# Performance work log

Measured on AMD Instinct MI355X. Metric: run time of the kernel, lower is better.

## Reference

```python
import jax, jax.numpy as jnp
import numpy as np

N = 100000
E = 3200000
IN_C, HID, OUT_C = 256, 32, 16


def gcn_conv(x, W, b, src, dst, n):
    """PyG GCNConv: h = D^{-1/2}(A+I)D^{-1/2} (x W) + b, self-loops already in src/dst."""
    h = x @ W  # [N, out]
    deg = jax.ops.segment_sum(jnp.ones_like(dst, dtype=h.dtype), dst, num_segments=n)
    dinv = jax.lax.rsqrt(deg)  # deg >= 1 because of self-loops
    norm = dinv[src] * dinv[dst]  # [E_all]
    msg = h[src] * norm[:, None]  # gather + normalize
    return jax.ops.segment_sum(msg, dst, num_segments=n) + b


def setup_inputs() -> dict:
    key = jax.random.key(0)
    k1, k2, k3, k4 = jax.random.split(key, 4)
    x = jax.random.normal(k1, (N, IN_C), dtype=jnp.float32)
    edge_index = jax.random.randint(k2, (2, E), 0, N, dtype=jnp.int64)
    # Glorot-ish init for weights, zero bias (as in PyG defaults)
    W1 = jax.random.normal(k3, (IN_C, HID), dtype=jnp.float32) / np.sqrt(IN_C)
    b1 = jnp.zeros((HID,), dtype=jnp.float32)
    W2 = jax.random.normal(k4, (HID, OUT_C), dtype=jnp.float32) / np.sqrt(HID)
    b2 = jnp.zeros((OUT_C,), dtype=jnp.float32)
    return {"x": x, "edge_index": edge_index, "W1": W1, "b1": b1, "W2": W2, "b2": b2}


def reference(x, edge_index, W1, b1, W2, b2):
    n = x.shape[0]
    loops = jnp.arange(n, dtype=edge_index.dtype)
    src = jnp.concatenate([edge_index[0], loops])  # add self-loops
    dst = jnp.concatenate([edge_index[1], loops])
    h = jax.nn.relu(gcn_conv(x, W1, b1, src, dst, n))
    return gcn_conv(h, W2, b2, src, dst, n)
```

## Files before the change

### kernel.cpp

```cpp
#include <hip/hip_runtime.h>

#define IN_C 256
#define HIDC 32
#define OUTC 16
#define NPB  256
#define MAXBKT 800
#define CAP  16384
#define EPB  12288

typedef __attribute__((ext_vector_type(8))) short short8;
typedef __attribute__((ext_vector_type(4))) float f32x4;
union S8U4 { short8 s; unsigned u[4]; };

__device__ __forceinline__ unsigned bf16pair(float a, float b) {
    unsigned ua = __float_as_uint(a); ua += 0x7FFF + ((ua >> 16) & 1);
    unsigned ub = __float_as_uint(b); ub += 0x7FFF + ((ub >> 16) & 1);
    return (ua >> 16) | (ub & 0xFFFF0000u);
}
__device__ __forceinline__ float bf16lo(unsigned u) { return __uint_as_float(u << 16); }
__device__ __forceinline__ float bf16hi(unsigned u) { return __uint_as_float(u & 0xFFFF0000u); }
__device__ __forceinline__ unsigned rbf(float a) {
    unsigned u = __float_as_uint(a);
    u += 0x7FFF + ((u >> 16) & 1);
    return u >> 16;
}
__device__ __forceinline__ void split8(const float* xf, short8& hi, short8& lo) {
    S8U4 H, L;
#pragma unroll
    for (int i = 0; i < 4; ++i) {
        float a = xf[2 * i], b = xf[2 * i + 1];
        unsigned ha = rbf(a), hb = rbf(b);
        float ra = a - __uint_as_float(ha << 16);
        float rb = b - __uint_as_float(hb << 16);
        H.u[i] = ha | (hb << 16);
        L.u[i] = rbf(ra) | (rbf(rb) << 16);
    }
    hi = H.s; lo = L.s;
}

__device__ __forceinline__ int edge_at(const int* __restrict__ ei, long long idx, int is64) {
    return is64 ? ei[idx << 1] : ei[idx];
}

__global__ void k_detect(const int* __restrict__ ei, int* __restrict__ flag,
                         int* __restrict__ bkt_cur, int nbkt) {
    __shared__ int nz;
    if (threadIdx.x == 0) nz = 0;
    __syncthreads();
    if (ei[2 * threadIdx.x + 1] != 0) atomicOr(&nz, 1);
    for (int i = threadIdx.x; i < nbkt; i += 256) bkt_cur[i] = i * CAP;
    __syncthreads();
    if (threadIdx.x == 0) *flag = (nz == 0) ? 1 : 0;
}

__global__ __launch_bounds__(1024) void k_bin_scatter(const int* __restrict__ ei, long long E,
                                                      const int* __restrict__ flag,
                                                      int* __restrict__ bkt_cur,
                                                      unsigned* __restrict__ packed, int nbkt) {
    __shared__ unsigned ecw[EPB];
    __shared__ unsigned short ecb[EPB];
    __shared__ int hist[MAXBKT];
    int is64 = *flag;
    for (int i = threadIdx.x; i < nbkt; i += 1024) hist[i] = 0;
    __syncthreads();
    long long lo = (long long)blockIdx.x * EPB;
    int m = (int)((E - lo) < EPB ? (E - lo) : EPB);
    for (int i = threadIdx.x; i < m; i += 1024) {
        int s = edge_at(ei, lo + i, is64);
        int d = edge_at(ei, E + lo + i, is64);
        ecw[i] = (unsigned)s | ((unsigned)(d & (NPB - 1)) << 20);
        ecb[i] = (unsigned short)(d >> 8);
        atomicAdd(&hist[d >> 8], 1);
    }
    __syncthreads();
    for (int b = threadIdx.x; b < nbkt; b += 1024) {
        int c = hist[b];
        hist[b] = c ? atomicAdd(&bkt_cur[b], c) : 0;
    }
    __syncthreads();
    for (int i = threadIdx.x; i < m; i += 1024) {
        int slot = atomicAdd(&hist[ecb[i]], 1);
        packed[slot] = ecw[i];
    }
}

__global__ __launch_bounds__(256) void k_bucket_csr(const unsigned* __restrict__ packed,
                                                    const int* __restrict__ bkt_cur,
                                                    int* __restrict__ csr_src,
                                                    int* __restrict__ ptr,
                                                    int* __restrict__ cnt,
                                                    float* __restrict__ dinv, int n) {
    __shared__ int hist[NPB];
    __shared__ int off[NPB];
    hist[threadIdx.x] = 0;
    __syncthreads();
    int base = blockIdx.x * CAP;
    int m = bkt_cur[blockIdx.x] - base;
    for (int i = threadIdx.x; i < m; i += 256)
        atomicAdd(&hist[packed[base + i] >> 20], 1);
    __syncthreads();
    off[threadIdx.x] = hist[threadIdx.x];
    __syncthreads();
    for (int o = 1; o < NPB; o <<= 1) {
        int v = (threadIdx.x >= o) ? off[threadIdx.x - o] : 0;
        __syncthreads();
        off[threadIdx.x] += v;
        __syncthreads();
    }
    int node = blockIdx.x * NPB + threadIdx.x;
    {
        int exc = off[threadIdx.x] - hist[threadIdx.x];
        if (node < n) {
            ptr[node]  = base + exc;
            cnt[node]  = hist[threadIdx.x];
            dinv[node] = rsqrtf((float)hist[threadIdx.x] + 1.0f);
        }
        hist[threadIdx.x] = exc;
    }
    __syncthreads();
    for (int i = threadIdx.x; i < m; i += 256) {
        unsigned w = packed[base + i];
        int r = atomicAdd(&hist[w >> 20], 1);
        csr_src[base + r] = (int)(w & 0xFFFFF);
    }
}

__global__ void k_wfrag(const float* __restrict__ W1, unsigned short* __restrict__ wf) {
    int idx = blockIdx.x * 256 + threadIdx.x;
    if (idx >= 8 * 2 * 2 * 64) return;
    int lane = idx & 63;
    int part = (idx >> 6) & 1;
    int tile = (idx >> 7) & 1;
    int s    = idx >> 8;
    int col = tile * 16 + (lane & 15);
    int k0  = s * 32 + (lane >> 4) * 8;
#pragma unroll
    for (int j = 0; j < 8; ++j) {
        float v = W1[(long long)(k0 + j) * HIDC + col];
        unsigned h = rbf(v);
        float r = v - __uint_as_float(h << 16);
        wf[(long long)idx * 8 + j] = (unsigned short)(part == 0 ? h : rbf(r));
    }
}

__global__ __launch_bounds__(256) void k_gemm1(const float* __restrict__ x,
                                               const unsigned short* __restrict__ wf,
                                               const float* __restrict__ dinv,
                                               unsigned short* __restrict__ h1b_us, int n) {
    const int t = threadIdx.x;
    const int l = t & 63;
    const int w = t >> 6;
    const long long nb0 = (long long)blockIdx.x * 64 + w * 16;
    const int arow = l & 15;
    const int kg = l >> 4;
    const long long nodeA = nb0 + arow;
    const bool loadA = nodeA < n;
    f32x4 acc0 = {0.f, 0.f, 0.f, 0.f}, acc1 = {0.f, 0.f, 0.f, 0.f};

#pragma unroll
    for (int s = 0; s < 8; ++s) {
        float xf[8];
        if (loadA) {
            float4 v0 = *(const float4*)(x + nodeA * IN_C + s * 32 + kg * 8);
            float4 v1 = *(const float4*)(x + nodeA * IN_C + s * 32 + kg * 8 + 4);
            xf[0] = v0.x; xf[1] = v0.y; xf[2] = v0.z; xf[3] = v0.w;
            xf[4] = v1.x; xf[5] = v1.y; xf[6] = v1.z; xf[7] = v1.w;
        } else {
#pragma unroll
            for (int j = 0; j < 8; ++j) xf[j] = 0.f;
        }
        short8 ah, al;
        split8(xf, ah, al);
        const unsigned short* base = wf + ((long long)(s * 4) * 64 + l) * 8;
        short8 bh0 = *(const short8*)(base);
        short8 bl0 = *(const short8*)(base + 64 * 8);
        short8 bh1 = *(const short8*)(base + 2 * 64 * 8);
        short8 bl1 = *(const short8*)(base + 3 * 64 * 8);
        acc0 = __builtin_amdgcn_mfma_f32_16x16x32_bf16(ah, bh0, acc0, 0, 0, 0);
        acc0 = __builtin_amdgcn_mfma_f32_16x16x32_bf16(ah, bl0, acc0, 0, 0, 0);
        acc0 = __builtin_amdgcn_mfma_f32_16x16x32_bf16(al, bh0, acc0, 0, 0, 0);
        acc1 = __builtin_amdgcn_mfma_f32_16x16x32_bf16(ah, bh1, acc1, 0, 0, 0);
        acc1 = __builtin_amdgcn_mfma_f32_16x16x32_bf16(ah, bl1, acc1, 0, 0, 0);
        acc1 = __builtin_amdgcn_mfma_f32_16x16x32_bf16(al, bh1, acc1, 0, 0, 0);
    }
#pragma unroll
    for (int r = 0; r < 4; ++r) {
        long long nd = nb0 + (l >> 4) * 4 + r;
        if (nd < n) {
            float di = dinv[nd];
            h1b_us[nd * 32 + (l & 15)]      = (unsigned short)rbf(acc0[r] * di);
            h1b_us[nd * 32 + 16 + (l & 15)] = (unsigned short)rbf(acc1[r] * di);
        }
    }
}

__global__ __launch_bounds__(256) void k_agg1csr(const int* __restrict__ ptr,
                                                 const int* __restrict__ cnt,
                                                 const int* __restrict__ csr_src,
                                                 const float* __restrict__ dinv,
                                                 const unsigned* __restrict__ h1b,
                                                 const float* __restrict__ b1,
                                                 float* __restrict__ h1r, int n) {
    long long g = (long long)blockIdx.x * blockDim.x + threadIdx.x;
    int node = (int)(g >> 4);
    int cp = (int)(g & 15);
    if (node >= n) return;
    unsigned us = h1b[(long long)node * 16 + cp];
    float accL = bf16lo(us), accH = bf16hi(us);
    int st = ptr[node], deg = cnt[node];
    int j = 0;
    for (; j + 3 < deg; j += 4) {
        int s0 = csr_src[st + j], s1 = csr_src[st + j + 1];
        int s2 = csr_src[st + j + 2], s3 = csr_src[st + j + 3];
        unsigned u0 = h1b[(long long)s0 * 16 + cp];
        unsigned u1 = h1b[(long long)s1 * 16 + cp];
        unsigned u2 = h1b[(long long)s2 * 16 + cp];
        unsigned u3 = h1b[(long long)s3 * 16 + cp];
        accL += (bf16lo(u0) + bf16lo(u1)) + (bf16lo(u2) + bf16lo(u3));
        accH += (bf16hi(u0) + bf16hi(u1)) + (bf16hi(u2) + bf16hi(u3));
    }
    for (; j < deg; ++j) {
        unsigned u = h1b[(long long)csr_src[st + j] * 16 + cp];
        accL += bf16lo(u); accH += bf16hi(u);
    }
    float di = dinv[node];
    float vL = accL * di + b1[2 * cp];
    float vH = accH * di + b1[2 * cp + 1];
    *(float2*)(h1r + (long long)node * HIDC + 2 * cp) =
        make_float2(vL > 0.f ? vL : 0.f, vH > 0.f ? vH : 0.f);
}

__global__ __launch_bounds__(256) void k_gemm2(const float* __restrict__ h1,
                                               const float* __restrict__ W2,
                                               const float* __restrict__ dinv,
                                               unsigned* __restrict__ h2b, int n) {
    const int t = threadIdx.x;
    const int oq = (t & 3) * 4;
    const long long node = (long long)blockIdx.x * 64 + (t >> 2);
    if (node >= n) return;
    const float* __restrict__ xp = h1 + node * HIDC;
    float a0 = 0.f, a1 = 0.f, a2 = 0.f, a3 = 0.f;
#pragma unroll
    for (int k0 = 0; k0 < HIDC; k0 += 8) {
        float4 xv0 = *(const float4*)(xp + k0);
        float4 xv1 = *(const float4*)(xp + k0 + 4);
        const float* __restrict__ wp = W2 + (long long)k0 * OUTC + oq;
        float4 w0 = *(const float4*)(wp + 0 * OUTC);
        float4 w1 = *(const float4*)(wp + 1 * OUTC);
        float4 w2 = *(const float4*)(wp + 2 * OUTC);
        float4 w3 = *(const float4*)(wp + 3 * OUTC);
        float4 w4 = *(const float4*)(wp + 4 * OUTC);
        float4 w5 = *(const float4*)(wp + 5 * OUTC);
        float4 w6 = *(const float4*)(wp + 6 * OUTC);
        float4 w7 = *(const float4*)(wp + 7 * OUTC);
        a0 = fmaf(xv0.x, w0.x, a0); a1 = fmaf(xv0.x, w0.y, a1);
        a2 = fmaf(xv0.x, w0.z, a2); a3 = fmaf(xv0.x, w0.w, a3);
        a0 = fmaf(xv0.y, w1.x, a0); a1 = fmaf(xv0.y, w1.y, a1);
        a2 = fmaf(xv0.y, w1.z, a2); a3 = fmaf(xv0.y, w1.w, a3);
        a0 = fmaf(xv0.z, w2.x, a0); a1 = fmaf(xv0.z, w2.y, a1);
        a2 = fmaf(xv0.z, w2.z, a2); a3 = fmaf(xv0.z, w2.w, a3);
        a0 = fmaf(xv0.w, w3.x, a0); a1 = fmaf(xv0.w, w3.y, a1);
        a2 = fmaf(xv0.w, w3.z, a2); a3 = fmaf(xv0.w, w3.w, a3);
        a0 = fmaf(xv1.x, w4.x, a0); a1 = fmaf(xv1.x, w4.y, a1);
        a2 = fmaf(xv1.x, w4.z, a2); a3 = fmaf(xv1.x, w4.w, a3);
        a0 = fmaf(xv1.y, w5.x, a0); a1 = fmaf(xv1.y, w5.y, a1);
        a2 = fmaf(xv1.y, w5.z, a2); a3 = fmaf(xv1.y, w5.w, a3);
        a0 = fmaf(xv1.z, w6.x, a0); a1 = fmaf(xv1.z, w6.y, a1);
        a2 = fmaf(xv1.z, w6.z, a2); a3 = fmaf(xv1.z, w6.w, a3);
        a0 = fmaf(xv1.w, w7.x, a0); a1 = fmaf(xv1.w, w7.y, a1);
        a2 = fmaf(xv1.w, w7.z, a2); a3 = fmaf(xv1.w, w7.w, a3);
    }
    float di = dinv[node];
    uint2 p;
    p.x = bf16pair(a0 * di, a1 * di);
    p.y = bf16pair(a2 * di, a3 * di);
    *(uint2*)(h2b + node * (OUTC / 2) + oq / 2) = p;
}

__global__ __launch_bounds__(256) void k_agg2csr(const int* __restrict__ ptr,
                                                 const int* __restrict__ cnt,
                                                 const int* __restrict__ csr_src,
                                                 const float* __restrict__ dinv,
                                                 const unsigned* __restrict__ h2b,
                                                 const float* __restrict__ b2,
                                                 float* __restrict__ out, int n) {
    long long g = (long long)blockIdx.x * blockDim.x + threadIdx.x;
    int node = (int)(g >> 3);
    int cp = (int)(g & 7);
    if (node >= n) return;
    unsigned us = h2b[(long long)node * 8 + cp];
    float accL = bf16lo(us), accH = bf16hi(us);
    int st = ptr[node], deg = cnt[node];
    int j = 0;
    for (; j + 3 < deg; j += 4) {
        int s0 = csr_src[st + j], s1 = csr_src[st + j + 1];
        int s2 = csr_src[st + j + 2], s3 = csr_src[st + j + 3];
        unsigned u0 = h2b[(long long)s0 * 8 + cp];
        unsigned u1 = h2b[(long long)s1 * 8 + cp];
        unsigned u2 = h2b[(long long)s2 * 8 + cp];
        unsigned u3 = h2b[(long long)s3 * 8 + cp];
        accL += (bf16lo(u0) + bf16lo(u1)) + (bf16lo(u2) + bf16lo(u3));
        accH += (bf16hi(u0) + bf16hi(u1)) + (bf16hi(u2) + bf16hi(u3));
    }
    for (; j < deg; ++j) {
        unsigned u = h2b[(long long)csr_src[st + j] * 8 + cp];
        accL += bf16lo(u); accH += bf16hi(u);
    }
    float di = dinv[node];
    *(float2*)(out + (long long)node * OUTC + 2 * cp) =
        make_float2(accL * di + b2[2 * cp], accH * di + b2[2 * cp + 1]);
}

extern "C" void kernel_launch(void* const* d_in, const int* in_sizes, int n_in,
                              void* d_out, int out_size, void* d_ws, size_t ws_size,
                              hipStream_t stream) {
    const float* x  = (const float*)d_in[0];
    const int*   ei = (const int*)d_in[1];
    const float* W1 = (const float*)d_in[2];
    const float* b1 = (const float*)d_in[3];
    const float* W2 = (const float*)d_in[4];
    const float* b2 = (const float*)d_in[5];
    const int n = in_sizes[0] / IN_C;
    const long long E = in_sizes[1] / 2;
    float* out = (float*)d_out;

    const int nbkt = (n + NPB - 1) / NPB;

    char* ws = (char*)d_ws;
    size_t off = 0;
    auto alloc = [&](size_t bytes) { void* p = ws + off; off += (bytes + 255) & ~(size_t)255; return p; };
    int*      flag     = (int*)alloc(256);
    int*      bkt_cur  = (int*)alloc((size_t)MAXBKT * 4);
    float*    dinv     = (float*)alloc((size_t)n * 4);
    int*      cnt      = (int*)alloc((size_t)n * 4);
    int*      ptr      = (int*)alloc((size_t)n * 4);
    unsigned* packed   = (unsigned*)alloc((size_t)nbkt * CAP * 4);
    int*      csr_src  = (int*)alloc((size_t)nbkt * CAP * 4);
    unsigned short* wf = (unsigned short*)alloc(8 * 2 * 2 * 64 * 8 * 2);
    unsigned* h1b      = (unsigned*)alloc((size_t)n * (HIDC / 2) * 4);
    float*    h1r      = (float*)alloc((size_t)n * HIDC * 4);
    unsigned* h2b      = (unsigned*)alloc((size_t)n * (OUTC / 2) * 4);

    k_detect<<<1, 256, 0, stream>>>(ei, flag, bkt_cur, nbkt);
    k_wfrag<<<8, 256, 0, stream>>>(W1, wf);
    k_bin_scatter<<<(int)((E + EPB - 1) / EPB), 1024, 0, stream>>>(ei, E, flag, bkt_cur, packed, nbkt);
    k_bucket_csr<<<nbkt, NPB, 0, stream>>>(packed, bkt_cur, csr_src, ptr, cnt, dinv, n);

    k_gemm1<<<(n + 63) / 64, 256, 0, stream>>>(x, wf, dinv, (unsigned short*)h1b, n);
    k_agg1csr<<<(int)(((long long)n * 16 + 255) / 256), 256, 0, stream>>>(
        ptr, cnt, csr_src, dinv, h1b, b1, h1r, n);
    k_gemm2<<<(n + 63) / 64, 256, 0, stream>>>(h1r, W2, dinv, h2b, n);
    k_agg2csr<<<(int)(((long long)n * 8 + 255) / 256), 256, 0, stream>>>(
        ptr, cnt, csr_src, dinv, h2b, b2, out, n);
}
```

Measured before the change: 177.0 us.

## Fuse layer-1 aggregation with layer-2 GEMM and keep binned edges in registers

Merges the first-layer CSR aggregation and the second small GEMM into one kernel: aggregated ReLU rows are staged in shared memory and multiplied by W2, also held in shared memory. This removes the fp32 h1r round trip through global memory and one kernel launch. Separately, the binning scatter kernel now keeps each thread's 12 edges in registers instead of large shared-memory arrays, which frees LDS and may raise occupancy. The cost is extra registers and a block barrier in the fused kernel, and only half the threads do the GEMM step.

```diff
diff --git a/kernel.cpp b/kernel.cpp
--- a/kernel.cpp
+++ b/kernel.cpp
@@ -7,6 +7,7 @@
 #define MAXBKT 800
 #define CAP  16384
 #define EPB  12288
+#define EPT  12
 
 typedef __attribute__((ext_vector_type(8))) short short8;
 typedef __attribute__((ext_vector_type(4))) float f32x4;
@@ -57,20 +58,25 @@
                                                       const int* __restrict__ flag,
                                                       int* __restrict__ bkt_cur,
                                                       unsigned* __restrict__ packed, int nbkt) {
-    __shared__ unsigned ecw[EPB];
-    __shared__ unsigned short ecb[EPB];
     __shared__ int hist[MAXBKT];
     int is64 = *flag;
     for (int i = threadIdx.x; i < nbkt; i += 1024) hist[i] = 0;
     __syncthreads();
     long long lo = (long long)blockIdx.x * EPB;
     int m = (int)((E - lo) < EPB ? (E - lo) : EPB);
-    for (int i = threadIdx.x; i < m; i += 1024) {
-        int s = edge_at(ei, lo + i, is64);
-        int d = edge_at(ei, E + lo + i, is64);
-        ecw[i] = (unsigned)s | ((unsigned)(d & (NPB - 1)) << 20);
-        ecb[i] = (unsigned short)(d >> 8);
-        atomicAdd(&hist[d >> 8], 1);
+    unsigned ew[EPT];
+    int      eb[EPT];
+#pragma unroll
+    for (int j = 0; j < EPT; ++j) {
+        int i = j * 1024 + (int)threadIdx.x;
+        eb[j] = -1;
+        if (i < m) {
+            int s = edge_at(ei, lo + i, is64);
+            int d = edge_at(ei, E + lo + i, is64);
+            ew[j] = (unsigned)s | ((unsigned)(d & (NPB - 1)) << 20);
+            eb[j] = d >> 8;
+            atomicAdd(&hist[eb[j]], 1);
+        }
     }
     __syncthreads();
     for (int b = threadIdx.x; b < nbkt; b += 1024) {
@@ -78,9 +84,12 @@
         hist[b] = c ? atomicAdd(&bkt_cur[b], c) : 0;
     }
     __syncthreads();
-    for (int i = threadIdx.x; i < m; i += 1024) {
-        int slot = atomicAdd(&hist[ecb[i]], 1);
-        packed[slot] = ecw[i];
+#pragma unroll
+    for (int j = 0; j < EPT; ++j) {
+        if (eb[j] >= 0) {
+            int slot = atomicAdd(&hist[eb[j]], 1);
+            packed[slot] = ew[j];
+        }
     }
 }
 
@@ -194,87 +203,66 @@
     }
 }
 
-__global__ __launch_bounds__(256) void k_agg1csr(const int* __restrict__ ptr,
-                                                 const int* __restrict__ cnt,
-                                                 const int* __restrict__ csr_src,
-                                                 const float* __restrict__ dinv,
-                                                 const unsigned* __restrict__ h1b,
-                                                 const float* __restrict__ b1,
-                                                 float* __restrict__ h1r, int n) {
-    long long g = (long long)blockIdx.x * blockDim.x + threadIdx.x;
-    int node = (int)(g >> 4);
-    int cp = (int)(g & 15);
-    if (node >= n) return;
-    unsigned us = h1b[(long long)node * 16 + cp];
-    float accL = bf16lo(us), accH = bf16hi(us);
-    int st = ptr[node], deg = cnt[node];
-    int j = 0;
-    for (; j + 3 < deg; j += 4) {
-        int s0 = csr_src[st + j], s1 = csr_src[st + j + 1];
-        int s2 = csr_src[st + j + 2], s3 = csr_src[st + j + 3];
-        unsigned u0 = h1b[(long long)s0 * 16 + cp];
-        unsigned u1 = h1b[(long long)s1 * 16 + cp];
-        unsigned u2 = h1b[(long long)s2 * 16 + cp];
-        unsigned u3 = h1b[(long long)s3 * 16 + cp];
-        accL += (bf16lo(u0) + bf16lo(u1)) + (bf16lo(u2) + bf16lo(u3));
-        accH += (bf16hi(u0) + bf16hi(u1)) + (bf16hi(u2) + bf16hi(u3));
-    }
-    for (; j < deg; ++j) {
-        unsigned u = h1b[(long long)csr_src[st + j] * 16 + cp];
-        accL += bf16lo(u); accH += bf16hi(u);
-    }
-    float di = dinv[node];
-    float vL = accL * di + b1[2 * cp];
-    float vH = accH * di + b1[2 * cp + 1];
-    *(float2*)(h1r + (long long)node * HIDC + 2 * cp) =
-        make_float2(vL > 0.f ? vL : 0.f, vH > 0.f ? vH : 0.f);
-}
-
-__global__ __launch_bounds__(256) void k_gemm2(const float* __restrict__ h1,
-                                               const float* __restrict__ W2,
-                                               const float* __restrict__ dinv,
-                                               unsigned* __restrict__ h2b, int n) {
+__global__ __launch_bounds__(256) void k_agg1g2(const int* __restrict__ ptr,
+                                                const int* __restrict__ cnt,
+                                                const int* __restrict__ csr_src,
+                                                const float* __restrict__ dinv,
+                                                const unsigned* __restrict__ h1b,
+                                                const float* __restrict__ b1,
+                                                const float* __restrict__ W2,
+                                                unsigned* __restrict__ h2b, int n) {
+    __shared__ float hs[16][33];
+    __shared__ float wl2[32][17];
     const int t = threadIdx.x;
-    const int oq = (t & 3) * 4;
-    const long long node = (long long)blockIdx.x * 64 + (t >> 2);
-    if (node >= n) return;
-    const float* __restrict__ xp = h1 + node * HIDC;
-    float a0 = 0.f, a1 = 0.f, a2 = 0.f, a3 = 0.f;
-#pragma unroll
-    for (int k0 = 0; k0 < HIDC; k0 += 8) {
-        float4 xv0 = *(const float4*)(xp + k0);
-        float4 xv1 = *(const float4*)(xp + k0 + 4);
-        const float* __restrict__ wp = W2 + (long long)k0 * OUTC + oq;
-        float4 w0 = *(const float4*)(wp + 0 * OUTC);
-        float4 w1 = *(const float4*)(wp + 1 * OUTC);
-        float4 w2 = *(const float4*)(wp + 2 * OUTC);
-        float4 w3 = *(const float4*)(wp + 3 * OUTC);
-        float4 w4 = *(const float4*)(wp + 4 * OUTC);
-        float4 w5 = *(const float4*)(wp + 5 * OUTC);
-        float4 w6 = *(const float4*)(wp + 6 * OUTC);
-        float4 w7 = *(const float4*)(wp + 7 * OUTC);
-        a0 = fmaf(xv0.x, w0.x, a0); a1 = fmaf(xv0.x, w0.y, a1);
-        a2 = fmaf(xv0.x, w0.z, a2); a3 = fmaf(xv0.x, w0.w, a3);
-        a0 = fmaf(xv0.y, w1.x, a0); a1 = fmaf(xv0.y, w1.y, a1);
-        a2 = fmaf(xv0.y, w1.z, a2); a3 = fmaf(xv0.y, w1.w, a3);
-        a0 = fmaf(xv0.z, w2.x, a0); a1 = fmaf(xv0.z, w2.y, a1);
-        a2 = fmaf(xv0.z, w2.z, a2); a3 = fmaf(xv0.z, w2.w, a3);
-        a0 = fmaf(xv0.w, w3.x, a0); a1 = fmaf(xv0.w, w3.y, a1);
-        a2 = fmaf(xv0.w, w3.z, a2); a3 = fmaf(xv0.w, w3.w, a3);
-        a0 = fmaf(xv1.x, w4.x, a0); a1 = fmaf(xv1.x, w4.y, a1);
-        a2 = fmaf(xv1.x, w4.z, a2); a3 = fmaf(xv1.x, w4.w, a3);
-        a0 = fmaf(xv1.y, w5.x, a0); a1 = fmaf(xv1.y, w5.y, a1);
-        a2 = fmaf(xv1.y, w5.z, a2); a3 = fmaf(xv1.y, w5.w, a3);
-        a0 = fmaf(xv1.z, w6.x, a0); a1 = fmaf(xv1.z, w6.y, a1);
-        a2 = fmaf(xv1.z, w6.z, a2); a3 = fmaf(xv1.z, w6.w, a3);
-        a0 = fmaf(xv1.w, w7.x, a0); a1 = fmaf(xv1.w, w7.y, a1);
-        a2 = fmaf(xv1.w, w7.z, a2); a3 = fmaf(xv1.w, w7.w, a3);
-    }
-    float di = dinv[node];
-    uint2 p;
-    p.x = bf16pair(a0 * di, a1 * di);
-    p.y = bf16pair(a2 * di, a3 * di);
-    *(uint2*)(h2b + node * (OUTC / 2) + oq / 2) = p;
+    for (int i = t; i < HIDC * OUTC; i += 256) wl2[i >> 4][i & 15] = W2[i];
+    const int nl = t >> 4;
+    const int cp = t & 15;
+    const long long node = (long long)blockIdx.x * 16 + nl;
+    float vL = 0.f, vH = 0.f;
+    if (node < n) {
+        unsigned us = h1b[node * 16 + cp];
+        float accL = bf16lo(us), accH = bf16hi(us);
+        int st = ptr[node], deg = cnt[node];
+        int j = 0;
+        for (; j + 3 < deg; j += 4) {
+            int s0 = csr_src[st + j], s1 = csr_src[st + j + 1];
+            int s2 = csr_src[st + j + 2], s3 = csr_src[st + j + 3];
+            unsigned u0 = h1b[(long long)s0 * 16 + cp];
+            unsigned u1 = h1b[(long long)s1 * 16 + cp];
+            unsigned u2 = h1b[(long long)s2 * 16 + cp];
+            unsigned u3 = h1b[(long long)s3 * 16 + cp];
+            accL += (bf16lo(u0) + bf16lo(u1)) + (bf16lo(u2) + bf16lo(u3));
+            accH += (bf16hi(u0) + bf16hi(u1)) + (bf16hi(u2) + bf16hi(u3));
+        }
+        for (; j < deg; ++j) {
+            unsigned u = h1b[(long long)csr_src[st + j] * 16 + cp];
+            accL += bf16lo(u); accH += bf16hi(u);
+        }
+        float di = dinv[node];
+        vL = accL * di + b1[2 * cp];
+        vH = accH * di + b1[2 * cp + 1];
+        vL = vL > 0.f ? vL : 0.f;
+        vH = vH > 0.f ? vH : 0.f;
+    }
+    hs[nl][2 * cp]     = vL;
+    hs[nl][2 * cp + 1] = vH;
+    __syncthreads();
+    if (t < 128) {
+        int nl2 = t >> 3;
+        int op  = t & 7;
+        long long nd = (long long)blockIdx.x * 16 + nl2;
+        if (nd < n) {
+            float o0 = 0.f, o1 = 0.f;
+#pragma unroll
+            for (int k = 0; k < HIDC; ++k) {
+                float h = hs[nl2][k];
+                o0 = fmaf(h, wl2[k][2 * op],     o0);
+                o1 = fmaf(h, wl2[k][2 * op + 1], o1);
+            }
+            float di = dinv[nd];
+            h2b[nd * 8 + op] = bf16pair(o0 * di, o1 * di);
+        }
+    }
 }
 
 __global__ __launch_bounds__(256) void k_agg2csr(const int* __restrict__ ptr,
@@ -338,7 +326,6 @@
     int*      csr_src  = (int*)alloc((size_t)nbkt * CAP * 4);
     unsigned short* wf = (unsigned short*)alloc(8 * 2 * 2 * 64 * 8 * 2);
     unsigned* h1b      = (unsigned*)alloc((size_t)n * (HIDC / 2) * 4);
-    float*    h1r      = (float*)alloc((size_t)n * HIDC * 4);
     unsigned* h2b      = (unsigned*)alloc((size_t)n * (OUTC / 2) * 4);
 
     k_detect<<<1, 256, 0, stream>>>(ei, flag, bkt_cur, nbkt);
@@ -347,9 +334,7 @@
     k_bucket_csr<<<nbkt, NPB, 0, stream>>>(packed, bkt_cur, csr_src, ptr, cnt, dinv, n);
 
     k_gemm1<<<(n + 63) / 64, 256, 0, stream>>>(x, wf, dinv, (unsigned short*)h1b, n);
-    k_agg1csr<<<(int)(((long long)n * 16 + 255) / 256), 256, 0, stream>>>(
-        ptr, cnt, csr_src, dinv, h1b, b1, h1r, n);
-    k_gemm2<<<(n + 63) / 64, 256, 0, stream>>>(h1r, W2, dinv, h2b, n);
+    k_agg1g2<<<(n + 15) / 16, 256, 0, stream>>>(ptr, cnt, csr_src, dinv, h1b, b1, W2, h2b, n);
     k_agg2csr<<<(int)(((long long)n * 8 + 255) / 256), 256, 0, stream>>>(
         ptr, cnt, csr_src, dinv, h2b, b2, out, n);
 }
```

Result: faster. 171.7 us (-3.0%).
